# Kernel optimization log

Hardware: AMD Instinct MI355X
Metric: run time of the kernel (lower is better)

The kernel has to match this reference:

```python
import jax, jax.numpy as jnp
import numpy as np

B, T, N, C = 4, 16, 50000, 16
E, DEG = 50000, 16
TOTAL = E * DEG
LAM = 0.3
COS_EPS = 1e-8   # torch cosine_similarity eps
NORM_EPS = 1e-8  # min-max normalization eps


def _build_window_dynamic_features(x_raw):
    # (B,T,N,C) -> (B,N,2C): per-node window mean and std as dynamic features
    mu = jnp.mean(x_raw, axis=1)
    sd = jnp.std(x_raw, axis=1)
    return jnp.concatenate([mu, sd], axis=-1)


def setup_inputs() -> dict:
    key = jax.random.key(0)
    k1, k2, k3, k4 = jax.random.split(key, 4)
    x_raw = jax.random.normal(k1, (B, T, N, C), dtype=jnp.float32)
    H = jnp.zeros((1, 1), dtype=jnp.float32)  # unused by forward; placeholder
    W = jax.random.uniform(k2, (E,), dtype=jnp.float32)
    edge_members = jax.random.randint(k3, (TOTAL,), 0, N, dtype=jnp.int32)
    edge_centers = jax.random.randint(k4, (E,), 0, N, dtype=jnp.int32)
    # CSR offsets, fixed degree DEG per hyperedge
    edge_offsets = jnp.arange(E + 1, dtype=jnp.int32) * DEG
    return {"x_raw": x_raw, "H": H, "W": W, "edge_members": edge_members,
            "edge_centers": edge_centers, "edge_offsets": edge_offsets}


def reference(x_raw, H, W, edge_members, edge_centers, edge_offsets):
    feat = _build_window_dynamic_features(x_raw)          # (B, N, D)
    E_ = W.shape[0]
    total = edge_members.shape[0]
    deg = edge_offsets[1:] - edge_offsets[:-1]            # (E,)
    member_edge_ids = jnp.repeat(jnp.arange(E_, dtype=jnp.int32), deg,
                                 total_repeat_length=total)  # (total,)

    member_feat = feat[:, edge_members, :]                       # (B, total, D)
    center_feat = feat[:, edge_centers[member_edge_ids], :]      # (B, total, D)

    # cosine similarity with torch-style eps clamping of norms
    dot = jnp.sum(member_feat * center_feat, axis=-1)            # (B, total)
    mn = jnp.maximum(jnp.linalg.norm(member_feat, axis=-1), COS_EPS)
    cn = jnp.maximum(jnp.linalg.norm(center_feat, axis=-1), COS_EPS)
    sim = jnp.clip(dot / (mn * cn), 0.0, 1.0)                    # (B, total)

    # segment scatter-add into per-edge bins, then mean
    sums = jax.ops.segment_sum(sim.T, member_edge_ids, num_segments=E_).T  # (B, E)
    counts = jnp.maximum(deg.astype(sim.dtype), 1.0)
    mean_sim = sums / counts[None, :]                            # (B, E)

    # per-batch min-max normalization
    smin = jnp.min(mean_sim, axis=1, keepdims=True)
    smax = jnp.max(mean_sim, axis=1, keepdims=True)
    mean_sim = (mean_sim - smin) / (smax - smin + NORM_EPS)

    return W[None, :] * (1.0 + LAM * mean_sim)                   # (B, E)
```

## Files before the change

kernel.cpp:

```cpp
#include <hip/hip_runtime.h>
#include <hip/hip_fp16.h>

#define Bn 4
#define Tn 16
#define Nn 50000
#define Cn 16
#define En 50000
#define LAM 0.3f
#define COS_EPS 1e-8f
#define NORM_EPS 1e-8f

union H8 { __half2 h2[4]; float4 f4; };

__global__ void feat_kernel(const float* __restrict__ x, float4* __restrict__ feat,
                            unsigned* __restrict__ mm) {
    if (blockIdx.x == 0 && threadIdx.x < 2 * Bn) {
        mm[threadIdx.x] = (threadIdx.x & 1) ? 0u : 0x7F800000u;
    }
    int gid = blockIdx.x * blockDim.x + threadIdx.x;
    if (gid >= Bn * Nn * 4) return;
    int c4 = gid & 3;
    int b  = (gid >> 2) & 3;
    int n  = gid >> 4;

    const float4* x4 = (const float4*)x;
    float4 s  = make_float4(0.f, 0.f, 0.f, 0.f);
    float4 ss = make_float4(0.f, 0.f, 0.f, 0.f);
    int base = (b * Tn) * Nn;
#pragma unroll
    for (int t = 0; t < Tn; ++t) {
        float4 v = x4[(base + t * Nn + n) * 4 + c4];
        s.x += v.x; s.y += v.y; s.z += v.z; s.w += v.w;
        ss.x += v.x * v.x; ss.y += v.y * v.y; ss.z += v.z * v.z; ss.w += v.w * v.w;
    }
    const float inv = 1.0f / (float)Tn;
    float4 m, sd;
    m.x = s.x * inv; m.y = s.y * inv; m.z = s.z * inv; m.w = s.w * inv;
    sd.x = sqrtf(fmaxf(ss.x * inv - m.x * m.x, 0.f));
    sd.y = sqrtf(fmaxf(ss.y * inv - m.y * m.y, 0.f));
    sd.z = sqrtf(fmaxf(ss.z * inv - m.z * m.z, 0.f));
    sd.w = sqrtf(fmaxf(ss.w * inv - m.w * m.w, 0.f));

    float p = m.x * m.x + m.y * m.y + m.z * m.z + m.w * m.w
            + sd.x * sd.x + sd.y * sd.y + sd.z * sd.z + sd.w * sd.w;
    p += __shfl_xor(p, 1);
    p += __shfl_xor(p, 2);
    float rn = 1.0f / fmaxf(sqrtf(p), COS_EPS);

    H8 o;
    o.h2[0] = __floats2half2_rn(m.x * rn,  m.y * rn);
    o.h2[1] = __floats2half2_rn(m.z * rn,  m.w * rn);
    o.h2[2] = __floats2half2_rn(sd.x * rn, sd.y * rn);
    o.h2[3] = __floats2half2_rn(sd.z * rn, sd.w * rn);
    feat[gid] = o.f4;
}

__global__ void edge_sim_kernel(const float4* __restrict__ feat,
                                const int* __restrict__ members,
                                const int* __restrict__ centers,
                                const int* __restrict__ offsets,
                                float* __restrict__ ms) {
    int tid  = blockIdx.x * blockDim.x + threadIdx.x;
    int e    = __builtin_amdgcn_readfirstlane(tid >> 6);
    if (e >= En) return;
    int lane = threadIdx.x & 63;
    int g    = lane >> 2;
    int q    = lane & 3;

    int off0 = offsets[e];
    int off1 = offsets[e + 1];
    int deg  = off1 - off0;
    int cn   = centers[e];

    int mn0 = (g < deg) ? members[off0 + g] : -1;

    H8 cp[Bn];
#pragma unroll
    for (int b_ = 0; b_ < Bn; ++b_) cp[b_].f4 = feat[(cn * 4 + b_) * 4 + q];

    float sums[Bn] = {0.f, 0.f, 0.f, 0.f};
    for (int m0 = g; m0 < deg; m0 += 16) {
        int mn = (m0 == g) ? mn0 : members[off0 + m0];
#pragma unroll
        for (int b_ = 0; b_ < Bn; ++b_) {
            H8 u; u.f4 = feat[(mn * 4 + b_) * 4 + q];
            float d = 0.f;
#pragma unroll
            for (int i = 0; i < 4; ++i) {
                float2 pm = __half22float2(u.h2[i]);
                float2 pc = __half22float2(cp[b_].h2[i]);
                d += pm.x * pc.x + pm.y * pc.y;
            }
            d += __shfl_xor(d, 1);
            d += __shfl_xor(d, 2);
            sums[b_] += fminf(fmaxf(d, 0.f), 1.f);
        }
    }
#pragma unroll
    for (int b_ = 0; b_ < Bn; ++b_) {
        float s = sums[b_];
        s += __shfl_xor(s, 4);
        s += __shfl_xor(s, 8);
        s += __shfl_xor(s, 16);
        s += __shfl_xor(s, 32);
        sums[b_] = s;
    }
    if (lane == 0) {
        float invd = 1.0f / fmaxf((float)deg, 1.0f);
#pragma unroll
        for (int b_ = 0; b_ < Bn; ++b_) ms[b_ * En + e] = sums[b_] * invd;
    }
}

__global__ void minmax_kernel(const float* __restrict__ ms, unsigned* __restrict__ mm) {
    int b = blockIdx.x >> 6;
    int j = blockIdx.x & 63;
    const float* p = ms + b * En;
    float lo = INFINITY, hi = 0.f;
    for (int i = j * blockDim.x + threadIdx.x; i < En; i += 64 * 256) {
        float v = p[i];
        lo = fminf(lo, v);
        hi = fmaxf(hi, v);
    }
#pragma unroll
    for (int m = 1; m < 64; m <<= 1) {
        lo = fminf(lo, __shfl_xor(lo, m));
        hi = fmaxf(hi, __shfl_xor(hi, m));
    }
    __shared__ float slo[4], shi[4];
    int wid  = threadIdx.x >> 6;
    int lane = threadIdx.x & 63;
    if (lane == 0) { slo[wid] = lo; shi[wid] = hi; }
    __syncthreads();
    if (threadIdx.x == 0) {
        float flo = fminf(fminf(slo[0], slo[1]), fminf(slo[2], slo[3]));
        float fhi = fmaxf(fmaxf(shi[0], shi[1]), fmaxf(shi[2], shi[3]));
        atomicMin(&mm[b * 2],     __float_as_uint(flo));
        atomicMax(&mm[b * 2 + 1], __float_as_uint(fhi));
    }
}

__global__ void out_kernel(const float* __restrict__ ms, const unsigned* __restrict__ mm,
                           const float* __restrict__ W, float* __restrict__ out) {
    int gid = blockIdx.x * blockDim.x + threadIdx.x;
    if (gid >= Bn * En) return;
    int b = gid / En;
    int e = gid - b * En;
    float smin = __uint_as_float(mm[b * 2]);
    float smax = __uint_as_float(mm[b * 2 + 1]);
    float v = (ms[gid] - smin) * __frcp_rn(smax - smin + NORM_EPS);
    out[gid] = W[e] * (1.0f + LAM * v);
}

extern "C" void kernel_launch(void* const* d_in, const int* in_sizes, int n_in,
                              void* d_out, int out_size, void* d_ws, size_t ws_size,
                              hipStream_t stream) {
    const float* x_raw        = (const float*)d_in[0];
    const float* W            = (const float*)d_in[2];
    const int*   edge_members = (const int*)d_in[3];
    const int*   edge_centers = (const int*)d_in[4];
    const int*   edge_offsets = (const int*)d_in[5];
    float*       out          = (float*)d_out;

    float4*   feat = (float4*)d_ws;
    float*    ms   = (float*)((char*)d_ws + (size_t)Nn * Bn * 64);
    unsigned* mm   = (unsigned*)(ms + (size_t)Bn * En);

    {
        int total = Bn * Nn * 4;
        feat_kernel<<<(total + 255) / 256, 256, 0, stream>>>(x_raw, feat, mm);
    }
    {
        long long threads = (long long)En * 64;
        int blocks = (int)((threads + 255) / 256);
        edge_sim_kernel<<<blocks, 256, 0, stream>>>(
            feat, edge_members, edge_centers, edge_offsets, ms);
    }
    minmax_kernel<<<Bn * 64, 256, 0, stream>>>(ms, mm);
    {
        int total = Bn * En;
        out_kernel<<<(total + 255) / 256, 256, 0, stream>>>(ms, mm, W, out);
    }
}
```

Measured before the change: 75.69 us.

## Fuse min-max reduction into edge kernel with slotted atomics, vectorize output

Removes the separate min-max kernel: each edge-sim block reduces its per-batch min and max in shared memory and atomically updates one of 64 spread slots per batch. The output kernel reduces the 64 slots per batch itself and then processes four elements per thread with float4 loads and stores. This drops one launch and one full reread of the mean-similarity buffer, at the cost of about 12.5k blocks issuing atomics into 256 slots per array and a block-wide barrier in the edge kernel.

```diff
diff --git a/kernel.cpp b/kernel.cpp
--- a/kernel.cpp
+++ b/kernel.cpp
@@ -13,9 +13,10 @@
 union H8 { __half2 h2[4]; float4 f4; };
 
 __global__ void feat_kernel(const float* __restrict__ x, float4* __restrict__ feat,
-                            unsigned* __restrict__ mm) {
-    if (blockIdx.x == 0 && threadIdx.x < 2 * Bn) {
-        mm[threadIdx.x] = (threadIdx.x & 1) ? 0u : 0x7F800000u;
+                            unsigned* __restrict__ pmin, unsigned* __restrict__ pmax) {
+    if (blockIdx.x == 0) {
+        pmin[threadIdx.x] = 0x7F800000u;
+        pmax[threadIdx.x] = 0u;
     }
     int gid = blockIdx.x * blockDim.x + threadIdx.x;
     if (gid >= Bn * Nn * 4) return;
@@ -59,97 +60,114 @@
                                 const int* __restrict__ members,
                                 const int* __restrict__ centers,
                                 const int* __restrict__ offsets,
-                                float* __restrict__ ms) {
+                                float* __restrict__ ms,
+                                unsigned* __restrict__ pmin,
+                                unsigned* __restrict__ pmax) {
     int tid  = blockIdx.x * blockDim.x + threadIdx.x;
     int e    = __builtin_amdgcn_readfirstlane(tid >> 6);
-    if (e >= En) return;
     int lane = threadIdx.x & 63;
+    int wid  = threadIdx.x >> 6;
     int g    = lane >> 2;
     int q    = lane & 3;
 
-    int off0 = offsets[e];
-    int off1 = offsets[e + 1];
-    int deg  = off1 - off0;
-    int cn   = centers[e];
-
-    int mn0 = (g < deg) ? members[off0 + g] : -1;
-
-    H8 cp[Bn];
-#pragma unroll
-    for (int b_ = 0; b_ < Bn; ++b_) cp[b_].f4 = feat[(cn * 4 + b_) * 4 + q];
-
-    float sums[Bn] = {0.f, 0.f, 0.f, 0.f};
-    for (int m0 = g; m0 < deg; m0 += 16) {
-        int mn = (m0 == g) ? mn0 : members[off0 + m0];
+    __shared__ float redlo[4][Bn], redhi[4][Bn];
+
+    if (e < En) {
+        int off0 = offsets[e];
+        int off1 = offsets[e + 1];
+        int deg  = off1 - off0;
+        int cn   = centers[e];
+
+        int mn0 = (g < deg) ? members[off0 + g] : -1;
+
+        H8 cp[Bn];
+#pragma unroll
+        for (int b_ = 0; b_ < Bn; ++b_) cp[b_].f4 = feat[(cn * 4 + b_) * 4 + q];
+
+        float sums[Bn] = {0.f, 0.f, 0.f, 0.f};
+        for (int m0 = g; m0 < deg; m0 += 16) {
+            int mn = (m0 == g) ? mn0 : members[off0 + m0];
+#pragma unroll
+            for (int b_ = 0; b_ < Bn; ++b_) {
+                H8 u; u.f4 = feat[(mn * 4 + b_) * 4 + q];
+                float d = 0.f;
+#pragma unroll
+                for (int i = 0; i < 4; ++i) {
+                    float2 pm = __half22float2(u.h2[i]);
+                    float2 pc = __half22float2(cp[b_].h2[i]);
+                    d += pm.x * pc.x + pm.y * pc.y;
+                }
+                d += __shfl_xor(d, 1);
+                d += __shfl_xor(d, 2);
+                sums[b_] += fminf(fmaxf(d, 0.f), 1.f);
+            }
+        }
 #pragma unroll
         for (int b_ = 0; b_ < Bn; ++b_) {
-            H8 u; u.f4 = feat[(mn * 4 + b_) * 4 + q];
-            float d = 0.f;
-#pragma unroll
-            for (int i = 0; i < 4; ++i) {
-                float2 pm = __half22float2(u.h2[i]);
-                float2 pc = __half22float2(cp[b_].h2[i]);
-                d += pm.x * pc.x + pm.y * pc.y;
+            float s = sums[b_];
+            s += __shfl_xor(s, 4);
+            s += __shfl_xor(s, 8);
+            s += __shfl_xor(s, 16);
+            s += __shfl_xor(s, 32);
+            sums[b_] = s;
+        }
+        if (lane == 0) {
+            float invd = 1.0f / fmaxf((float)deg, 1.0f);
+#pragma unroll
+            for (int b_ = 0; b_ < Bn; ++b_) {
+                float v = sums[b_] * invd;
+                ms[b_ * En + e] = v;
+                redlo[wid][b_] = v;
+                redhi[wid][b_] = v;
             }
-            d += __shfl_xor(d, 1);
-            d += __shfl_xor(d, 2);
-            sums[b_] += fminf(fmaxf(d, 0.f), 1.f);
-        }
-    }
-#pragma unroll
-    for (int b_ = 0; b_ < Bn; ++b_) {
-        float s = sums[b_];
-        s += __shfl_xor(s, 4);
-        s += __shfl_xor(s, 8);
-        s += __shfl_xor(s, 16);
-        s += __shfl_xor(s, 32);
-        sums[b_] = s;
-    }
-    if (lane == 0) {
-        float invd = 1.0f / fmaxf((float)deg, 1.0f);
-#pragma unroll
-        for (int b_ = 0; b_ < Bn; ++b_) ms[b_ * En + e] = sums[b_] * invd;
-    }
-}
-
-__global__ void minmax_kernel(const float* __restrict__ ms, unsigned* __restrict__ mm) {
-    int b = blockIdx.x >> 6;
-    int j = blockIdx.x & 63;
-    const float* p = ms + b * En;
-    float lo = INFINITY, hi = 0.f;
-    for (int i = j * blockDim.x + threadIdx.x; i < En; i += 64 * 256) {
-        float v = p[i];
-        lo = fminf(lo, v);
-        hi = fmaxf(hi, v);
-    }
-#pragma unroll
-    for (int m = 1; m < 64; m <<= 1) {
-        lo = fminf(lo, __shfl_xor(lo, m));
-        hi = fmaxf(hi, __shfl_xor(hi, m));
-    }
-    __shared__ float slo[4], shi[4];
-    int wid  = threadIdx.x >> 6;
-    int lane = threadIdx.x & 63;
-    if (lane == 0) { slo[wid] = lo; shi[wid] = hi; }
+        }
+    } else if (lane == 0) {
+#pragma unroll
+        for (int b_ = 0; b_ < Bn; ++b_) { redlo[wid][b_] = INFINITY; redhi[wid][b_] = 0.f; }
+    }
     __syncthreads();
-    if (threadIdx.x == 0) {
-        float flo = fminf(fminf(slo[0], slo[1]), fminf(slo[2], slo[3]));
-        float fhi = fmaxf(fmaxf(shi[0], shi[1]), fmaxf(shi[2], shi[3]));
-        atomicMin(&mm[b * 2],     __float_as_uint(flo));
-        atomicMax(&mm[b * 2 + 1], __float_as_uint(fhi));
-    }
-}
-
-__global__ void out_kernel(const float* __restrict__ ms, const unsigned* __restrict__ mm,
+    if (threadIdx.x < Bn) {
+        int b_ = threadIdx.x;
+        float mn = fminf(fminf(redlo[0][b_], redlo[1][b_]), fminf(redlo[2][b_], redlo[3][b_]));
+        float mx = fmaxf(fmaxf(redhi[0][b_], redhi[1][b_]), fmaxf(redhi[2][b_], redhi[3][b_]));
+        int slot = blockIdx.x & 63;
+        atomicMin(&pmin[b_ * 64 + slot], __float_as_uint(mn));
+        atomicMax(&pmax[b_ * 64 + slot], __float_as_uint(mx));
+    }
+}
+
+__global__ void out_kernel(const float* __restrict__ ms,
+                           const unsigned* __restrict__ pmin,
+                           const unsigned* __restrict__ pmax,
                            const float* __restrict__ W, float* __restrict__ out) {
-    int gid = blockIdx.x * blockDim.x + threadIdx.x;
-    if (gid >= Bn * En) return;
-    int b = gid / En;
-    int e = gid - b * En;
-    float smin = __uint_as_float(mm[b * 2]);
-    float smax = __uint_as_float(mm[b * 2 + 1]);
-    float v = (ms[gid] - smin) * __frcp_rn(smax - smin + NORM_EPS);
-    out[gid] = W[e] * (1.0f + LAM * v);
+    int b = blockIdx.y;
+    __shared__ float s_lo, s_hi;
+    if (threadIdx.x < 64) {
+        float lo = __uint_as_float(pmin[b * 64 + threadIdx.x]);
+        float hi = __uint_as_float(pmax[b * 64 + threadIdx.x]);
+#pragma unroll
+        for (int m = 1; m < 64; m <<= 1) {
+            lo = fminf(lo, __shfl_xor(lo, m));
+            hi = fmaxf(hi, __shfl_xor(hi, m));
+        }
+        if (threadIdx.x == 0) { s_lo = lo; s_hi = hi; }
+    }
+    __syncthreads();
+    float smin = s_lo;
+    float rcp  = __frcp_rn(s_hi - smin + NORM_EPS);
+
+    int i4 = blockIdx.x * blockDim.x + threadIdx.x;
+    if (i4 < En / 4) {
+        const float4* msp = (const float4*)(ms + (size_t)b * En);
+        const float4* Wp  = (const float4*)W;
+        float4 m4 = msp[i4], w4 = Wp[i4];
+        float4 o;
+        o.x = w4.x * (1.0f + LAM * ((m4.x - smin) * rcp));
+        o.y = w4.y * (1.0f + LAM * ((m4.y - smin) * rcp));
+        o.z = w4.z * (1.0f + LAM * ((m4.z - smin) * rcp));
+        o.w = w4.w * (1.0f + LAM * ((m4.w - smin) * rcp));
+        ((float4*)(out + (size_t)b * En))[i4] = o;
+    }
 }
 
 extern "C" void kernel_launch(void* const* d_in, const int* in_sizes, int n_in,
@@ -164,21 +182,21 @@
 
     float4*   feat = (float4*)d_ws;
     float*    ms   = (float*)((char*)d_ws + (size_t)Nn * Bn * 64);
-    unsigned* mm   = (unsigned*)(ms + (size_t)Bn * En);
+    unsigned* pmin = (unsigned*)(ms + (size_t)Bn * En);
+    unsigned* pmax = pmin + Bn * 64;
 
     {
         int total = Bn * Nn * 4;
-        feat_kernel<<<(total + 255) / 256, 256, 0, stream>>>(x_raw, feat, mm);
+        feat_kernel<<<(total + 255) / 256, 256, 0, stream>>>(x_raw, feat, pmin, pmax);
     }
     {
         long long threads = (long long)En * 64;
         int blocks = (int)((threads + 255) / 256);
         edge_sim_kernel<<<blocks, 256, 0, stream>>>(
-            feat, edge_members, edge_centers, edge_offsets, ms);
-    }
-    minmax_kernel<<<Bn * 64, 256, 0, stream>>>(ms, mm);
+            feat, edge_members, edge_centers, edge_offsets, ms, pmin, pmax);
+    }
     {
-        int total = Bn * En;
-        out_kernel<<<(total + 255) / 256, 256, 0, stream>>>(ms, mm, W, out);
-    }
-}
+        dim3 grid((En / 4 + 255) / 256, Bn);
+        out_kernel<<<grid, 256, 0, stream>>>(ms, pmin, pmax, W, out);
+    }
+}
```

Measured after the change: 105.5 us. 1.39x slower.
